# Performance work log

Hardware: AMD Instinct MI355X
Metric: run time of the kernel (lower is better)

Reference implementation:

```python
import jax, jax.numpy as jnp
import numpy as np

N, T, F_IN = 20000, 8, 64
FILTERS, HEADS = 32, 4
E = 320000
LEAKY = 0.2  # PyG GATConv default negative_slope
HID = HEADS * FILTERS  # 128


def setup_inputs() -> dict:
    key = jax.random.key(0)
    ks = jax.random.split(key, 16)
    g = lambda k, shape, scale: jax.random.normal(k, shape, dtype=jnp.float32) * scale
    return {
        "x": g(ks[0], (N, T, F_IN), 1.0),
        "edge_index": jax.random.randint(ks[1], (2, E), 0, N, dtype=jnp.int32),
        # GATConv 1: lin weight, attention vectors (per head), bias
        "W1": g(ks[2], (HID, F_IN), (2.0 / F_IN) ** 0.5),
        "att_src1": g(ks[3], (HEADS, FILTERS), 0.1),
        "att_dst1": g(ks[4], (HEADS, FILTERS), 0.1),
        "b1": jnp.zeros((HID,), jnp.float32),
        # GATConv 2
        "W2": g(ks[5], (HID, HID), (2.0 / HID) ** 0.5),
        "att_src2": g(ks[6], (HEADS, FILTERS), 0.1),
        "att_dst2": g(ks[7], (HEADS, FILTERS), 0.1),
        "b2": jnp.zeros((HID,), jnp.float32),
        # MLP head
        "lw1": g(ks[8], (FILTERS, HID), (2.0 / HID) ** 0.5),
        "lb1": jnp.zeros((FILTERS,), jnp.float32),
        "lw2": g(ks[9], (1, FILTERS), (2.0 / FILTERS) ** 0.5),
        "lb2": jnp.zeros((1,), jnp.float32),
    }


def gat_layer(x, src, dst, W, a_src, a_dst, b):
    """PyG GATConv (concat=True, add_self_loops already applied to src/dst)."""
    h = (x @ W.T).reshape(N, HEADS, FILTERS)          # [N,H,F]
    es = (h * a_src).sum(-1)                          # [N,H] per-node src score
    ed = (h * a_dst).sum(-1)                          # [N,H] per-node dst score
    e = jax.nn.leaky_relu(es[src] + ed[dst], LEAKY)   # [E',H]
    # segment softmax over incoming edges per destination node
    m = jax.ops.segment_max(e, dst, num_segments=N)
    ex = jnp.exp(e - m[dst])
    denom = jax.ops.segment_sum(ex, dst, num_segments=N)
    alpha = ex / (denom[dst] + 1e-16)                 # [E',H]
    out = jax.ops.segment_sum(h[src] * alpha[:, :, None], dst, num_segments=N)
    return out.reshape(N, HID) + b


def reference(x, edge_index, W1, att_src1, att_dst1, b1,
              W2, att_src2, att_dst2, b2, lw1, lb1, lw2, lb2):
    # add self loops (PyG GATConv default add_self_loops=True)
    loop = jnp.arange(N, dtype=edge_index.dtype)
    src = jnp.concatenate([edge_index[0], loop])
    dst = jnp.concatenate([edge_index[1], loop])

    def step(_, x_t):
        h = jax.nn.elu(gat_layer(x_t, src, dst, W1, att_src1, att_dst1, b1))
        # dropout is identity in eval mode
        h = jax.nn.elu(gat_layer(h, src, dst, W2, att_src2, att_dst2, b2))
        h = jax.nn.relu(h @ lw1.T + lb1)
        y = h @ lw2.T + lb2                            # [N,1]
        return None, y

    _, ys = jax.lax.scan(step, None, jnp.transpose(x, (1, 0, 2)))  # scan over T
    return ys  # [T, N, 1] (stacked version of the original list of outputs)
```

## Files before the change

### kernel.cpp

```cpp
#include <hip/hip_runtime.h>

constexpr int cN     = 20000;
constexpr int cT     = 8;
constexpr int cFIN   = 64;
constexpr int cHEADS = 4;
constexpr int cF     = 32;
constexpr int cHID   = 128;
constexpr int cE     = 320000;
constexpr int cET    = cE + cN;
constexpr int cR     = cN * cT;
constexpr float cLEAKY = 0.2f;
constexpr float cL2E = 1.44269504088896340736f;

typedef __attribute__((ext_vector_type(8))) short bf16x8;
typedef __attribute__((ext_vector_type(4))) float f32x4;

static __device__ __forceinline__ unsigned short f2bfu(float f) {
    unsigned int u;
    __builtin_memcpy(&u, &f, 4);
    u += 0x7FFFu + ((u >> 16) & 1u);
    return (unsigned short)(u >> 16);
}
static __device__ __forceinline__ void unpack2(unsigned int v, float& lo, float& hi) {
    unsigned int ul = v << 16, uh = v & 0xFFFF0000u;
    __builtin_memcpy(&lo, &ul, 4);
    __builtin_memcpy(&hi, &uh, 4);
}
static __device__ __forceinline__ unsigned int pack2(float lo, float hi) {
    unsigned int ul, uh;
    __builtin_memcpy(&ul, &lo, 4);
    __builtin_memcpy(&uh, &hi, 4);
    ul += 0x7FFFu + ((ul >> 16) & 1u);
    uh += 0x7FFFu + ((uh >> 16) & 1u);
    return (ul >> 16) | (uh & 0xFFFF0000u);
}

__global__ void cvt_w_kernel(const float* W1, const float* W2, const float* lw1,
                             unsigned short* W1b, unsigned short* W2b, unsigned short* lw1b) {
    int i = blockIdx.x * 256 + threadIdx.x;
    if (i < cHID * cFIN)                      W1b[i] = f2bfu(W1[i]);
    else if (i < cHID * cFIN + cHID * cHID)   W2b[i - cHID * cFIN] = f2bfu(W2[i - cHID * cFIN]);
    else if (i < cHID * cFIN + cHID * cHID + cF * cHID)
        lw1b[i - cHID * cFIN - cHID * cHID] = f2bfu(lw1[i - cHID * cFIN - cHID * cHID]);
}

__global__ void deg_init_kernel(int* deg) {
    int n = blockIdx.x * blockDim.x + threadIdx.x;
    if (n < cN) deg[n] = 1;
}
__global__ void deg_count_kernel(const int* ei, int* deg) {
    int e = blockIdx.x * blockDim.x + threadIdx.x;
    if (e < cE) atomicAdd(&deg[ei[cE + e]], 1);
}
__global__ void scan_kernel(const int* deg, int* offs, int* cur) {
    __shared__ int sdeg[79 * 256];
    __shared__ int lds[256];
    int tid = threadIdx.x;
    #pragma unroll 4
    for (int k = 0; k < 79; k++) {
        int idx = k * 256 + tid;
        sdeg[idx] = (idx < cN) ? deg[idx] : 0;
    }
    __syncthreads();
    const int CH = 79;
    int base = tid * CH;
    int tot = 0;
    #pragma unroll 8
    for (int j = 0; j < CH; j++) tot += sdeg[base + j];
    lds[tid] = tot;
    __syncthreads();
    for (int off = 1; off < 256; off <<= 1) {
        int v = (tid >= off) ? lds[tid - off] : 0;
        __syncthreads();
        lds[tid] += v;
        __syncthreads();
    }
    int run = lds[tid] - tot;
    for (int j = 0; j < CH; j++) {
        int idx = base + j;
        if (idx < cN) { offs[idx] = run; cur[idx] = run; run += sdeg[idx]; }
    }
    if (tid == 255) offs[cN] = lds[255];
}
__global__ void scatter_kernel(const int* ei, int* cur, int* csr) {
    int e = blockIdx.x * blockDim.x + threadIdx.x;
    if (e >= cET) return;
    int s, d;
    if (e < cE) { s = ei[e]; d = ei[cE + e]; }
    else        { s = e - cE; d = s; }
    int pos = atomicAdd(&cur[d], 1);
    csr[pos] = s;
}

__global__ __launch_bounds__(256) void gemm1_fused_kernel(
        const float* __restrict__ x, const unsigned short* __restrict__ W,
        const float* __restrict__ a_src, const float* __restrict__ a_dst,
        unsigned short* __restrict__ hb, float* __restrict__ es, float* __restrict__ ed) {
    __shared__ float hl[64][132];
    int tid  = threadIdx.x;
    int wave = tid >> 6;
    int lane = tid & 63;
    int q    = lane >> 4;
    int mi   = lane & 15;
    int m0   = blockIdx.x * 64 + wave * 16;

    int rho = m0 + mi;
    int t = rho / cN;
    int n = rho - t * cN;
    const float* xr = x + (size_t)n * (cT * cFIN) + t * cFIN;

    bf16x8 afrag[2];
    #pragma unroll
    for (int s = 0; s < 2; s++) {
        float4 v0 = *(const float4*)(xr + s * 32 + q * 8);
        float4 v1 = *(const float4*)(xr + s * 32 + q * 8 + 4);
        bf16x8 f;
        f[0] = (short)f2bfu(v0.x); f[1] = (short)f2bfu(v0.y);
        f[2] = (short)f2bfu(v0.z); f[3] = (short)f2bfu(v0.w);
        f[4] = (short)f2bfu(v1.x); f[5] = (short)f2bfu(v1.y);
        f[6] = (short)f2bfu(v1.z); f[7] = (short)f2bfu(v1.w);
        afrag[s] = f;
    }

    f32x4 acc[8];
    #pragma unroll
    for (int ct = 0; ct < 8; ct++) acc[ct] = (f32x4){0.f, 0.f, 0.f, 0.f};
    #pragma unroll
    for (int ct = 0; ct < 8; ct++) {
        int c = ct * 16 + mi;
        #pragma unroll
        for (int s = 0; s < 2; s++) {
            bf16x8 bfrag = *(const bf16x8*)(W + (size_t)c * cFIN + s * 32 + q * 8);
            acc[ct] = __builtin_amdgcn_mfma_f32_16x16x32_bf16(afrag[s], bfrag, acc[ct], 0, 0, 0);
        }
    }

    #pragma unroll
    for (int ct = 0; ct < 8; ct++)
        #pragma unroll
        for (int r = 0; r < 4; r++)
            hl[wave * 16 + q * 4 + r][ct * 16 + mi] = acc[ct][r];
    __syncthreads();

    {
        int r2 = tid & 63;
        int hd = tid >> 6;
        int rg = blockIdx.x * 64 + r2;
        const float* hr = &hl[r2][hd * cF];
        const float* sa = a_src + hd * cF;
        const float* da = a_dst + hd * cF;
        float s1 = 0.f, s2 = 0.f;
        #pragma unroll 8
        for (int f = 0; f < cF; f++) {
            float hv = hr[f];
            s1 += hv * sa[f];
            s2 += hv * da[f];
        }
        es[rg * cHEADS + hd] = s1 * cL2E;
        ed[rg * cHEADS + hd] = s2 * cL2E;
    }

    size_t base = (size_t)blockIdx.x * 64 * cHID;
    #pragma unroll
    for (int it = 0; it < 8; it++) {
        int g   = tid + it * 256;
        int row = g >> 5;
        int c4  = (g & 31) * 4;
        float4 v = *(const float4*)&hl[row][c4];
        unsigned int p0 = pack2(v.x, v.y), p1 = pack2(v.z, v.w);
        *(uint2*)(hb + base + (size_t)row * cHID + c4) = make_uint2(p0, p1);
    }
}

static __device__ __forceinline__ void agg_core(
        const unsigned short* __restrict__ hb, const float* __restrict__ es,
        const float* __restrict__ ed, const int* __restrict__ offs,
        const int* __restrict__ csr, const float* __restrict__ bias,
        int t, int n, int j, float* r) {
    int head = j >> 2;
    int rho  = t * cN + n;
    int s0 = offs[n], s1 = offs[n + 1];
    float edn = ed[(size_t)rho * cHEADS + head];
    const char* hpc = (const char*)(hb + (size_t)t * cN * cHID);
    const char* epc = (const char*)(es + (size_t)t * cN * cHEADS);
    const char* cc  = (const char*)csr;
    unsigned jo = (unsigned)j * 16u;
    unsigned ho = (unsigned)head * 4u;

    float acc[8] = {};
    float den = 0.f;
    int i = s0;
    for (; i + 3 < s1; i += 4) {
        unsigned io = (unsigned)i * 4u;
        int sa = *(const int*)(cc + io);
        int sb = *(const int*)(cc + io + 4u);
        int sc = *(const int*)(cc + io + 8u);
        int sd = *(const int*)(cc + io + 12u);
        uint4 ra = *(const uint4*)(hpc + (((unsigned)sa) << 8) + jo);
        uint4 rb = *(const uint4*)(hpc + (((unsigned)sb) << 8) + jo);
        uint4 rc = *(const uint4*)(hpc + (((unsigned)sc) << 8) + jo);
        uint4 rd = *(const uint4*)(hpc + (((unsigned)sd) << 8) + jo);
        float ea = *(const float*)(epc + (((unsigned)sa) << 4) + ho) + edn;
        float eb = *(const float*)(epc + (((unsigned)sb) << 4) + ho) + edn;
        float ec = *(const float*)(epc + (((unsigned)sc) << 4) + ho) + edn;
        float ee = *(const float*)(epc + (((unsigned)sd) << 4) + ho) + edn;
        ea = (ea >= 0.f) ? ea : cLEAKY * ea;
        eb = (eb >= 0.f) ? eb : cLEAKY * eb;
        ec = (ec >= 0.f) ? ec : cLEAKY * ec;
        ee = (ee >= 0.f) ? ee : cLEAKY * ee;
        float wa = __builtin_amdgcn_exp2f(ea), wb = __builtin_amdgcn_exp2f(eb);
        float wc = __builtin_amdgcn_exp2f(ec), wd = __builtin_amdgcn_exp2f(ee);
        den += wa; den += wb; den += wc; den += wd;
        float lo, hi;
        unpack2(ra.x, lo, hi); acc[0] += wa * lo; acc[1] += wa * hi;
        unpack2(ra.y, lo, hi); acc[2] += wa * lo; acc[3] += wa * hi;
        unpack2(ra.z, lo, hi); acc[4] += wa * lo; acc[5] += wa * hi;
        unpack2(ra.w, lo, hi); acc[6] += wa * lo; acc[7] += wa * hi;
        unpack2(rb.x, lo, hi); acc[0] += wb * lo; acc[1] += wb * hi;
        unpack2(rb.y, lo, hi); acc[2] += wb * lo; acc[3] += wb * hi;
        unpack2(rb.z, lo, hi); acc[4] += wb * lo; acc[5] += wb * hi;
        unpack2(rb.w, lo, hi); acc[6] += wb * lo; acc[7] += wb * hi;
        unpack2(rc.x, lo, hi); acc[0] += wc * lo; acc[1] += wc * hi;
        unpack2(rc.y, lo, hi); acc[2] += wc * lo; acc[3] += wc * hi;
        unpack2(rc.z, lo, hi); acc[4] += wc * lo; acc[5] += wc * hi;
        unpack2(rc.w, lo, hi); acc[6] += wc * lo; acc[7] += wc * hi;
        unpack2(rd.x, lo, hi); acc[0] += wd * lo; acc[1] += wd * hi;
        unpack2(rd.y, lo, hi); acc[2] += wd * lo; acc[3] += wd * hi;
        unpack2(rd.z, lo, hi); acc[4] += wd * lo; acc[5] += wd * hi;
        unpack2(rd.w, lo, hi); acc[6] += wd * lo; acc[7] += wd * hi;
    }
    for (; i < s1; i++) {
        int sa = *(const int*)(cc + (unsigned)i * 4u);
        uint4 ra = *(const uint4*)(hpc + (((unsigned)sa) << 8) + jo);
        float ea = *(const float*)(epc + (((unsigned)sa) << 4) + ho) + edn;
        ea = (ea >= 0.f) ? ea : cLEAKY * ea;
        float wa = __builtin_amdgcn_exp2f(ea);
        den += wa;
        float lo, hi;
        unpack2(ra.x, lo, hi); acc[0] += wa * lo; acc[1] += wa * hi;
        unpack2(ra.y, lo, hi); acc[2] += wa * lo; acc[3] += wa * hi;
        unpack2(ra.z, lo, hi); acc[4] += wa * lo; acc[5] += wa * hi;
        unpack2(ra.w, lo, hi); acc[6] += wa * lo; acc[7] += wa * hi;
    }
    float inv = 1.f / (den + 1e-16f);
    float4 b0 = *(const float4*)(bias + 8 * j);
    float4 b1v = *(const float4*)(bias + 8 * j + 4);
    float v0 = acc[0] * inv + b0.x;  r[0] = (v0 > 0.f) ? v0 : expm1f(v0);
    float v1 = acc[1] * inv + b0.y;  r[1] = (v1 > 0.f) ? v1 : expm1f(v1);
    float v2 = acc[2] * inv + b0.z;  r[2] = (v2 > 0.f) ? v2 : expm1f(v2);
    float v3 = acc[3] * inv + b0.w;  r[3] = (v3 > 0.f) ? v3 : expm1f(v3);
    float v4 = acc[4] * inv + b1v.x; r[4] = (v4 > 0.f) ? v4 : expm1f(v4);
    float v5 = acc[5] * inv + b1v.y; r[5] = (v5 > 0.f) ? v5 : expm1f(v5);
    float v6 = acc[6] * inv + b1v.z; r[6] = (v6 > 0.f) ? v6 : expm1f(v6);
    float v7 = acc[7] * inv + b1v.w; r[7] = (v7 > 0.f) ? v7 : expm1f(v7);
}

__global__ __launch_bounds__(256) void agg_gemm_kernel(
        const unsigned short* __restrict__ hb, const float* __restrict__ es,
        const float* __restrict__ ed, const int* __restrict__ offs,
        const int* __restrict__ csr, const float* __restrict__ bias,
        const unsigned short* __restrict__ W2, const float* __restrict__ a_src,
        const float* __restrict__ a_dst, unsigned short* __restrict__ hb2,
        float* __restrict__ es2, float* __restrict__ ed2) {
    __shared__ unsigned short tile[16 * 128];
    __shared__ float hl[16][132];
    int b    = blockIdx.x;
    int t    = b & 7;
    int g    = b >> 3;
    int tid  = threadIdx.x;
    int lrow = tid >> 4;
    int j    = tid & 15;
    int n0   = g * 16;

    float r[8];
    agg_core(hb, es, ed, offs, csr, bias, t, n0 + lrow, j, r);
    {
        uint4 o;
        o.x = pack2(r[0], r[1]); o.y = pack2(r[2], r[3]);
        o.z = pack2(r[4], r[5]); o.w = pack2(r[6], r[7]);
        unsigned tb = (unsigned)lrow * 256u + (((unsigned)j * 16u) ^ (((unsigned)(lrow & 7)) << 4));
        *(uint4*)((char*)tile + tb) = o;
    }
    __syncthreads();

    int wave = tid >> 6;
    int lane = tid & 63;
    int q    = lane >> 4;
    int mi   = lane & 15;
    bf16x8 afrag[4];
    #pragma unroll
    for (int s = 0; s < 4; s++) {
        unsigned addr = (unsigned)mi * 256u +
                        (((unsigned)(s * 64 + q * 16)) ^ (((unsigned)(mi & 7)) << 4));
        afrag[s] = *(const bf16x8*)((const char*)tile + addr);
    }
    f32x4 acc2[2];
    acc2[0] = (f32x4){0.f, 0.f, 0.f, 0.f};
    acc2[1] = (f32x4){0.f, 0.f, 0.f, 0.f};
    #pragma unroll
    for (int ct = 0; ct < 2; ct++) {
        int c = (wave * 2 + ct) * 16 + mi;
        #pragma unroll
        for (int s = 0; s < 4; s++) {
            bf16x8 bfrag = *(const bf16x8*)(W2 + (size_t)c * cHID + s * 32 + q * 8);
            acc2[ct] = __builtin_amdgcn_mfma_f32_16x16x32_bf16(afrag[s], bfrag, acc2[ct], 0, 0, 0);
        }
    }
    #pragma unroll
    for (int ct = 0; ct < 2; ct++)
        #pragma unroll
        for (int rr = 0; rr < 4; rr++)
            hl[q * 4 + rr][(wave * 2 + ct) * 16 + mi] = acc2[ct][rr];
    __syncthreads();

    if (tid < 64) {
        int r2 = tid & 15;
        int hd = tid >> 4;
        int rg = t * cN + n0 + r2;
        const float* hr = &hl[r2][hd * cF];
        const float* sa = a_src + hd * cF;
        const float* da = a_dst + hd * cF;
        float s1 = 0.f, s2 = 0.f;
        #pragma unroll 8
        for (int f = 0; f < cF; f++) {
            float hv = hr[f];
            s1 += hv * sa[f];
            s2 += hv * da[f];
        }
        es2[(size_t)rg * cHEADS + hd] = s1 * cL2E;
        ed2[(size_t)rg * cHEADS + hd] = s2 * cL2E;
    }
    {
        int row = tid >> 4;
        int c8  = (tid & 15) * 8;
        float4 v0 = *(const float4*)&hl[row][c8];
        float4 v1 = *(const float4*)&hl[row][c8 + 4];
        uint4 o;
        o.x = pack2(v0.x, v0.y); o.y = pack2(v0.z, v0.w);
        o.z = pack2(v1.x, v1.y); o.w = pack2(v1.z, v1.w);
        *(uint4*)(hb2 + (size_t)(t * cN + n0 + row) * cHID + c8) = o;
    }
}

__global__ __launch_bounds__(256) void TemporalGAT_20005957665499_kernel(
        const unsigned short* __restrict__ hb2, const float* __restrict__ es,
        const float* __restrict__ ed, const int* __restrict__ offs,
        const int* __restrict__ csr, const float* __restrict__ bias,
        const unsigned short* __restrict__ lw1b, const float* __restrict__ lb1,
        const float* __restrict__ lw2, const float* __restrict__ lb2,
        float* __restrict__ out) {
    __shared__ unsigned short tile[16 * 128];
    int b    = blockIdx.x;
    int t    = b & 7;
    int g    = b >> 3;
    int tid  = threadIdx.x;
    int lrow = tid >> 4;
    int j    = tid & 15;
    int n0   = g * 16;

    float r[8];
    agg_core(hb2, es, ed, offs, csr, bias, t, n0 + lrow, j, r);
    {
        uint4 o;
        o.x = pack2(r[0], r[1]); o.y = pack2(r[2], r[3]);
        o.z = pack2(r[4], r[5]); o.w = pack2(r[6], r[7]);
        unsigned tb = (unsigned)lrow * 256u + (((unsigned)j * 16u) ^ (((unsigned)(lrow & 7)) << 4));
        *(uint4*)((char*)tile + tb) = o;
    }
    __syncthreads();

    if (tid < 64) {
        int q  = tid >> 4;
        int mi = tid & 15;
        bf16x8 afrag[4];
        #pragma unroll
        for (int s = 0; s < 4; s++) {
            unsigned addr = (unsigned)mi * 256u +
                            (((unsigned)(s * 64 + q * 16)) ^ (((unsigned)(mi & 7)) << 4));
            afrag[s] = *(const bf16x8*)((const char*)tile + addr);
        }
        f32x4 acc2[2];
        acc2[0] = (f32x4){0.f, 0.f, 0.f, 0.f};
        acc2[1] = (f32x4){0.f, 0.f, 0.f, 0.f};
        #pragma unroll
        for (int ct = 0; ct < 2; ct++) {
            int c = ct * 16 + mi;
            #pragma unroll
            for (int s = 0; s < 4; s++) {
                bf16x8 bfrag = *(const bf16x8*)(lw1b + (size_t)c * cHID + s * 32 + q * 8);
                acc2[ct] = __builtin_amdgcn_mfma_f32_16x16x32_bf16(afrag[s], bfrag, acc2[ct], 0, 0, 0);
            }
        }
        float lb1a = lb1[mi], lb1b_ = lb1[16 + mi];
        float lw2a = lw2[mi], lw2b_ = lw2[16 + mi];
        float l2 = lb2[0];
        #pragma unroll
        for (int rr = 0; rr < 4; rr++) {
            float va = fmaxf(acc2[0][rr] + lb1a, 0.f);
            float vb = fmaxf(acc2[1][rr] + lb1b_, 0.f);
            float v = va * lw2a + vb * lw2b_;
            v += __shfl_xor(v, 1);
            v += __shfl_xor(v, 2);
            v += __shfl_xor(v, 4);
            v += __shfl_xor(v, 8);
            if (mi == 0) out[t * cN + n0 + q * 4 + rr] = v + l2;
        }
    }
}

extern "C" void kernel_launch(void* const* d_in, const int* in_sizes, int n_in,
                              void* d_out, int out_size, void* d_ws, size_t ws_size,
                              hipStream_t stream) {
    const float* x   = (const float*)d_in[0];
    const int*   ei  = (const int*)d_in[1];
    const float* W1  = (const float*)d_in[2];
    const float* as1 = (const float*)d_in[3];
    const float* ad1 = (const float*)d_in[4];
    const float* b1  = (const float*)d_in[5];
    const float* W2  = (const float*)d_in[6];
    const float* as2 = (const float*)d_in[7];
    const float* ad2 = (const float*)d_in[8];
    const float* b2  = (const float*)d_in[9];
    const float* lw1 = (const float*)d_in[10];
    const float* lb1 = (const float*)d_in[11];
    const float* lw2 = (const float*)d_in[12];
    const float* lb2 = (const float*)d_in[13];
    float* out = (float*)d_out;
    (void)in_sizes; (void)n_in; (void)out_size; (void)ws_size;

    char* ws = (char*)d_ws;
    size_t o = 0;
    auto carveN = [&](size_t bytes) { void* p = ws + o; o += (bytes + 255) & ~(size_t)255; return p; };
    unsigned short* hb   = (unsigned short*)carveN((size_t)cR * cHID * 2);
    unsigned short* hb2  = (unsigned short*)carveN((size_t)cR * cHID * 2);
    unsigned short* W1b  = (unsigned short*)carveN((size_t)cHID * cFIN * 2);
    unsigned short* W2b  = (unsigned short*)carveN((size_t)cHID * cHID * 2);
    unsigned short* lw1b = (unsigned short*)carveN((size_t)cF * cHID * 2);
    float* es1_buf = (float*)carveN((size_t)cR * cHEADS * 4);
    float* ed1_buf = (float*)carveN((size_t)cR * cHEADS * 4);
    float* es2_buf = (float*)carveN((size_t)cR * cHEADS * 4);
    float* ed2_buf = (float*)carveN((size_t)cR * cHEADS * 4);
    int*   deg     = (int*)carveN((size_t)cN * 4);
    int*   offs    = (int*)carveN((size_t)(cN + 1) * 4);
    int*   cursor  = (int*)carveN((size_t)cN * 4);
    int*   csr     = (int*)carveN((size_t)cET * 4);

    cvt_w_kernel<<<(cHID * cFIN + cHID * cHID + cF * cHID + 255) / 256, 256, 0, stream>>>(
        W1, W2, lw1, W1b, W2b, lw1b);

    deg_init_kernel<<<(cN + 255) / 256, 256, 0, stream>>>(deg);
    deg_count_kernel<<<(cE + 255) / 256, 256, 0, stream>>>(ei, deg);
    scan_kernel<<<1, 256, 0, stream>>>(deg, offs, cursor);
    scatter_kernel<<<(cET + 255) / 256, 256, 0, stream>>>(ei, cursor, csr);

    gemm1_fused_kernel<<<cR / 64, 256, 0, stream>>>(x, W1b, as1, ad1, hb, es1_buf, ed1_buf);
    agg_gemm_kernel<<<(cN / 16) * cT, 256, 0, stream>>>(
        hb, es1_buf, ed1_buf, offs, csr, b1, W2b, as2, ad2, hb2, es2_buf, ed2_buf);
    TemporalGAT_20005957665499_kernel<<<(cN / 16) * cT, 256, 0, stream>>>(
        hb2, es2_buf, ed2_buf, offs, csr, b2, lw1b, lb1, lw2, lb2, out);
}
```

Before: 382.8 us.

## Aggregate 16 features per thread with 32-node blocks and merge setup kernels

```diff
diff --git a/kernel.cpp b/kernel.cpp
--- a/kernel.cpp
+++ b/kernel.cpp
@@ -14,6 +14,7 @@
 
 typedef __attribute__((ext_vector_type(8))) short bf16x8;
 typedef __attribute__((ext_vector_type(4))) float f32x4;
+typedef __attribute__((ext_vector_type(2))) float f32x2;
 
 static __device__ __forceinline__ unsigned short f2bfu(float f) {
     unsigned int u;
@@ -21,10 +22,12 @@
     u += 0x7FFFu + ((u >> 16) & 1u);
     return (unsigned short)(u >> 16);
 }
-static __device__ __forceinline__ void unpack2(unsigned int v, float& lo, float& hi) {
+static __device__ __forceinline__ f32x2 bfp2(unsigned int v) {
     unsigned int ul = v << 16, uh = v & 0xFFFF0000u;
+    float lo, hi;
     __builtin_memcpy(&lo, &ul, 4);
     __builtin_memcpy(&hi, &uh, 4);
+    return (f32x2){lo, hi};
 }
 static __device__ __forceinline__ unsigned int pack2(float lo, float hi) {
     unsigned int ul, uh;
@@ -34,24 +37,25 @@
     uh += 0x7FFFu + ((uh >> 16) & 1u);
     return (ul >> 16) | (uh & 0xFFFF0000u);
 }
-
-__global__ void cvt_w_kernel(const float* W1, const float* W2, const float* lw1,
-                             unsigned short* W1b, unsigned short* W2b, unsigned short* lw1b) {
+static __device__ __forceinline__ void fma16(uint4 r0, uint4 r1, float w, f32x2* acc) {
+    f32x2 w2 = (f32x2){w, w};
+    acc[0] += w2 * bfp2(r0.x); acc[1] += w2 * bfp2(r0.y);
+    acc[2] += w2 * bfp2(r0.z); acc[3] += w2 * bfp2(r0.w);
+    acc[4] += w2 * bfp2(r1.x); acc[5] += w2 * bfp2(r1.y);
+    acc[6] += w2 * bfp2(r1.z); acc[7] += w2 * bfp2(r1.w);
+}
+
+__global__ void cvt_deg_kernel(const float* W1, const float* W2, const float* lw1,
+                               const int* ei, unsigned short* W1b, unsigned short* W2b,
+                               unsigned short* lw1b, int* deg) {
     int i = blockIdx.x * 256 + threadIdx.x;
     if (i < cHID * cFIN)                      W1b[i] = f2bfu(W1[i]);
     else if (i < cHID * cFIN + cHID * cHID)   W2b[i - cHID * cFIN] = f2bfu(W2[i - cHID * cFIN]);
     else if (i < cHID * cFIN + cHID * cHID + cF * cHID)
         lw1b[i - cHID * cFIN - cHID * cHID] = f2bfu(lw1[i - cHID * cFIN - cHID * cHID]);
-}
-
-__global__ void deg_init_kernel(int* deg) {
-    int n = blockIdx.x * blockDim.x + threadIdx.x;
-    if (n < cN) deg[n] = 1;
-}
-__global__ void deg_count_kernel(const int* ei, int* deg) {
-    int e = blockIdx.x * blockDim.x + threadIdx.x;
-    if (e < cE) atomicAdd(&deg[ei[cE + e]], 1);
-}
+    if (i < cE) atomicAdd(&deg[ei[cE + i]], 1);
+}
+
 __global__ void scan_kernel(const int* deg, int* offs, int* cur) {
     __shared__ int sdeg[79 * 256];
     __shared__ int lds[256];
@@ -59,7 +63,7 @@
     #pragma unroll 4
     for (int k = 0; k < 79; k++) {
         int idx = k * 256 + tid;
-        sdeg[idx] = (idx < cN) ? deg[idx] : 0;
+        sdeg[idx] = (idx < cN) ? deg[idx] + 1 : 0;
     }
     __syncthreads();
     const int CH = 79;
@@ -172,87 +176,78 @@
     }
 }
 
-static __device__ __forceinline__ void agg_core(
+static __device__ __forceinline__ void agg_core16(
         const unsigned short* __restrict__ hb, const float* __restrict__ es,
         const float* __restrict__ ed, const int* __restrict__ offs,
         const int* __restrict__ csr, const float* __restrict__ bias,
         int t, int n, int j, float* r) {
-    int head = j >> 2;
-    int rho  = t * cN + n;
+    int head = j >> 1;
     int s0 = offs[n], s1 = offs[n + 1];
-    float edn = ed[(size_t)rho * cHEADS + head];
-    const char* hpc = (const char*)(hb + (size_t)t * cN * cHID);
-    const char* epc = (const char*)(es + (size_t)t * cN * cHEADS);
-    const char* cc  = (const char*)csr;
-    unsigned jo = (unsigned)j * 16u;
+    float edn = ed[(size_t)(t * cN + n) * cHEADS + head];
+    const char* hp = (const char*)(hb + (size_t)t * cN * cHID);
+    const char* ep = (const char*)(es + (size_t)t * cN * cHEADS);
+    const char* cc = (const char*)csr;
+    unsigned jo = (unsigned)j * 32u;
     unsigned ho = (unsigned)head * 4u;
 
-    float acc[8] = {};
+    f32x2 acc[8];
+    #pragma unroll
+    for (int k = 0; k < 8; k++) acc[k] = (f32x2){0.f, 0.f};
     float den = 0.f;
     int i = s0;
-    for (; i + 3 < s1; i += 4) {
+    for (; i + 1 < s1; i += 2) {
         unsigned io = (unsigned)i * 4u;
         int sa = *(const int*)(cc + io);
         int sb = *(const int*)(cc + io + 4u);
-        int sc = *(const int*)(cc + io + 8u);
-        int sd = *(const int*)(cc + io + 12u);
-        uint4 ra = *(const uint4*)(hpc + (((unsigned)sa) << 8) + jo);
-        uint4 rb = *(const uint4*)(hpc + (((unsigned)sb) << 8) + jo);
-        uint4 rc = *(const uint4*)(hpc + (((unsigned)sc) << 8) + jo);
-        uint4 rd = *(const uint4*)(hpc + (((unsigned)sd) << 8) + jo);
-        float ea = *(const float*)(epc + (((unsigned)sa) << 4) + ho) + edn;
-        float eb = *(const float*)(epc + (((unsigned)sb) << 4) + ho) + edn;
-        float ec = *(const float*)(epc + (((unsigned)sc) << 4) + ho) + edn;
-        float ee = *(const float*)(epc + (((unsigned)sd) << 4) + ho) + edn;
+        unsigned oa = ((unsigned)sa) << 8, ob = ((unsigned)sb) << 8;
+        uint4 ra0 = *(const uint4*)(hp + oa + jo);
+        uint4 ra1 = *(const uint4*)(hp + oa + jo + 16u);
+        uint4 rb0 = *(const uint4*)(hp + ob + jo);
+        uint4 rb1 = *(const uint4*)(hp + ob + jo + 16u);
+        float ea = *(const float*)(ep + (((unsigned)sa) << 4) + ho) + edn;
+        float eb = *(const float*)(ep + (((unsigned)sb) << 4) + ho) + edn;
         ea = (ea >= 0.f) ? ea : cLEAKY * ea;
         eb = (eb >= 0.f) ? eb : cLEAKY * eb;
-        ec = (ec >= 0.f) ? ec : cLEAKY * ec;
-        ee = (ee >= 0.f) ? ee : cLEAKY * ee;
-        float wa = __builtin_amdgcn_exp2f(ea), wb = __builtin_amdgcn_exp2f(eb);
-        float wc = __builtin_amdgcn_exp2f(ec), wd = __builtin_amdgcn_exp2f(ee);
-        den += wa; den += wb; den += wc; den += wd;
-        float lo, hi;
-        unpack2(ra.x, lo, hi); acc[0] += wa * lo; acc[1] += wa * hi;
-        unpack2(ra.y, lo, hi); acc[2] += wa * lo; acc[3] += wa * hi;
-        unpack2(ra.z, lo, hi); acc[4] += wa * lo; acc[5] += wa * hi;
-        unpack2(ra.w, lo, hi); acc[6] += wa * lo; acc[7] += wa * hi;
-        unpack2(rb.x, lo, hi); acc[0] += wb * lo; acc[1] += wb * hi;
-        unpack2(rb.y, lo, hi); acc[2] += wb * lo; acc[3] += wb * hi;
-        unpack2(rb.z, lo, hi); acc[4] += wb * lo; acc[5] += wb * hi;
-        unpack2(rb.w, lo, hi); acc[6] += wb * lo; acc[7] += wb * hi;
-        unpack2(rc.x, lo, hi); acc[0] += wc * lo; acc[1] += wc * hi;
-        unpack2(rc.y, lo, hi); acc[2] += wc * lo; acc[3] += wc * hi;
-        unpack2(rc.z, lo, hi); acc[4] += wc * lo; acc[5] += wc * hi;
-        unpack2(rc.w, lo, hi); acc[6] += wc * lo; acc[7] += wc * hi;
-        unpack2(rd.x, lo, hi); acc[0] += wd * lo; acc[1] += wd * hi;
-        unpack2(rd.y, lo, hi); acc[2] += wd * lo; acc[3] += wd * hi;
-        unpack2(rd.z, lo, hi); acc[4] += wd * lo; acc[5] += wd * hi;
-        unpack2(rd.w, lo, hi); acc[6] += wd * lo; acc[7] += wd * hi;
+        float wa = __builtin_amdgcn_exp2f(ea);
+        float wb = __builtin_amdgcn_exp2f(eb);
+        den += wa; den += wb;
+        fma16(ra0, ra1, wa, acc);
+        fma16(rb0, rb1, wb, acc);
     }
     for (; i < s1; i++) {
         int sa = *(const int*)(cc + (unsigned)i * 4u);
-        uint4 ra = *(const uint4*)(hpc + (((unsigned)sa) << 8) + jo);
-        float ea = *(const float*)(epc + (((unsigned)sa) << 4) + ho) + edn;
+        unsigned oa = ((unsigned)sa) << 8;
+        uint4 ra0 = *(const uint4*)(hp + oa + jo);
+        uint4 ra1 = *(const uint4*)(hp + oa + jo + 16u);
+        float ea = *(const float*)(ep + (((unsigned)sa) << 4) + ho) + edn;
         ea = (ea >= 0.f) ? ea : cLEAKY * ea;
         float wa = __builtin_amdgcn_exp2f(ea);
         den += wa;
-        float lo, hi;
-        unpack2(ra.x, lo, hi); acc[0] += wa * lo; acc[1] += wa * hi;
-        unpack2(ra.y, lo, hi); acc[2] += wa * lo; acc[3] += wa * hi;
-        unpack2(ra.z, lo, hi); acc[4] += wa * lo; acc[5] += wa * hi;
-        unpack2(ra.w, lo, hi); acc[6] += wa * lo; acc[7] += wa * hi;
+        fma16(ra0, ra1, wa, acc);
     }
     float inv = 1.f / (den + 1e-16f);
-    float4 b0 = *(const float4*)(bias + 8 * j);
-    float4 b1v = *(const float4*)(bias + 8 * j + 4);
-    float v0 = acc[0] * inv + b0.x;  r[0] = (v0 > 0.f) ? v0 : expm1f(v0);
-    float v1 = acc[1] * inv + b0.y;  r[1] = (v1 > 0.f) ? v1 : expm1f(v1);
-    float v2 = acc[2] * inv + b0.z;  r[2] = (v2 > 0.f) ? v2 : expm1f(v2);
-    float v3 = acc[3] * inv + b0.w;  r[3] = (v3 > 0.f) ? v3 : expm1f(v3);
-    float v4 = acc[4] * inv + b1v.x; r[4] = (v4 > 0.f) ? v4 : expm1f(v4);
-    float v5 = acc[5] * inv + b1v.y; r[5] = (v5 > 0.f) ? v5 : expm1f(v5);
-    float v6 = acc[6] * inv + b1v.z; r[6] = (v6 > 0.f) ? v6 : expm1f(v6);
-    float v7 = acc[7] * inv + b1v.w; r[7] = (v7 > 0.f) ? v7 : expm1f(v7);
+    const float* bp = bias + 16 * j;
+    #pragma unroll
+    for (int k = 0; k < 8; k++) {
+        float v0 = acc[k].x * inv + bp[2 * k];
+        float v1 = acc[k].y * inv + bp[2 * k + 1];
+        r[2 * k]     = (v0 > 0.f) ? v0 : expm1f(v0);
+        r[2 * k + 1] = (v1 > 0.f) ? v1 : expm1f(v1);
+    }
+}
+
+static __device__ __forceinline__ void tile_write16(unsigned short* tile, int row, int j,
+                                                    const float* r) {
+    uint4 o0, o1;
+    o0.x = pack2(r[0], r[1]);  o0.y = pack2(r[2], r[3]);
+    o0.z = pack2(r[4], r[5]);  o0.w = pack2(r[6], r[7]);
+    o1.x = pack2(r[8], r[9]);  o1.y = pack2(r[10], r[11]);
+    o1.z = pack2(r[12], r[13]); o1.w = pack2(r[14], r[15]);
+    unsigned swz = ((unsigned)(row & 7)) << 4;
+    unsigned jo  = (unsigned)j * 32u;
+    char* base = (char*)tile + (unsigned)row * 256u;
+    *(uint4*)(base + (jo ^ swz)) = o0;
+    *(uint4*)(base + ((jo + 16u) ^ swz)) = o1;
 }
 
 __global__ __launch_bounds__(256) void agg_gemm_kernel(
@@ -262,44 +257,41 @@
         const unsigned short* __restrict__ W2, const float* __restrict__ a_src,
         const float* __restrict__ a_dst, unsigned short* __restrict__ hb2,
         float* __restrict__ es2, float* __restrict__ ed2) {
-    __shared__ unsigned short tile[16 * 128];
-    __shared__ float hl[16][132];
+    __shared__ unsigned short tile[32 * 128];
+    __shared__ float hl[2][16][132];
     int b    = blockIdx.x;
     int t    = b & 7;
     int g    = b >> 3;
     int tid  = threadIdx.x;
-    int lrow = tid >> 4;
-    int j    = tid & 15;
-    int n0   = g * 16;
-
-    float r[8];
-    agg_core(hb, es, ed, offs, csr, bias, t, n0 + lrow, j, r);
-    {
-        uint4 o;
-        o.x = pack2(r[0], r[1]); o.y = pack2(r[2], r[3]);
-        o.z = pack2(r[4], r[5]); o.w = pack2(r[6], r[7]);
-        unsigned tb = (unsigned)lrow * 256u + (((unsigned)j * 16u) ^ (((unsigned)(lrow & 7)) << 4));
-        *(uint4*)((char*)tile + tb) = o;
-    }
+    int row  = tid >> 3;
+    int j    = tid & 7;
+    int n0   = g * 32;
+    int n    = n0 + row;
+
+    float r[16];
+    agg_core16(hb, es, ed, offs, csr, bias, t, n, j, r);
+    tile_write16(tile, row, j, r);
     __syncthreads();
 
     int wave = tid >> 6;
     int lane = tid & 63;
     int q    = lane >> 4;
     int mi   = lane & 15;
+    int p    = wave >> 1;
+    int ch   = wave & 1;
     bf16x8 afrag[4];
     #pragma unroll
     for (int s = 0; s < 4; s++) {
-        unsigned addr = (unsigned)mi * 256u +
+        unsigned addr = (unsigned)(p * 16 + mi) * 256u +
                         (((unsigned)(s * 64 + q * 16)) ^ (((unsigned)(mi & 7)) << 4));
         afrag[s] = *(const bf16x8*)((const char*)tile + addr);
     }
-    f32x4 acc2[2];
-    acc2[0] = (f32x4){0.f, 0.f, 0.f, 0.f};
-    acc2[1] = (f32x4){0.f, 0.f, 0.f, 0.f};
-    #pragma unroll
-    for (int ct = 0; ct < 2; ct++) {
-        int c = (wave * 2 + ct) * 16 + mi;
+    f32x4 acc2[4];
+    #pragma unroll
+    for (int ct = 0; ct < 4; ct++) acc2[ct] = (f32x4){0.f, 0.f, 0.f, 0.f};
+    #pragma unroll
+    for (int ct = 0; ct < 4; ct++) {
+        int c = (ch * 4 + ct) * 16 + mi;
         #pragma unroll
         for (int s = 0; s < 4; s++) {
             bf16x8 bfrag = *(const bf16x8*)(W2 + (size_t)c * cHID + s * 32 + q * 8);
@@ -307,17 +299,18 @@
         }
     }
     #pragma unroll
-    for (int ct = 0; ct < 2; ct++)
+    for (int ct = 0; ct < 4; ct++)
         #pragma unroll
         for (int rr = 0; rr < 4; rr++)
-            hl[q * 4 + rr][(wave * 2 + ct) * 16 + mi] = acc2[ct][rr];
-    __syncthreads();
-
-    if (tid < 64) {
+            hl[p][q * 4 + rr][(ch * 4 + ct) * 16 + mi] = acc2[ct][rr];
+    __syncthreads();
+
+    if (tid < 128) {
+        int pp = tid >> 6;
         int r2 = tid & 15;
-        int hd = tid >> 4;
-        int rg = t * cN + n0 + r2;
-        const float* hr = &hl[r2][hd * cF];
+        int hd = (tid >> 4) & 3;
+        int rg = t * cN + n0 + pp * 16 + r2;
+        const float* hr = &hl[pp][r2][hd * cF];
         const float* sa = a_src + hd * cF;
         const float* da = a_dst + hd * cF;
         float s1 = 0.f, s2 = 0.f;
@@ -330,15 +323,16 @@
         es2[(size_t)rg * cHEADS + hd] = s1 * cL2E;
         ed2[(size_t)rg * cHEADS + hd] = s2 * cL2E;
     }
-    {
-        int row = tid >> 4;
-        int c8  = (tid & 15) * 8;
-        float4 v0 = *(const float4*)&hl[row][c8];
-        float4 v1 = *(const float4*)&hl[row][c8 + 4];
+    #pragma unroll
+    for (int pp = 0; pp < 2; pp++) {
+        int rw = tid >> 4;
+        int c8 = (tid & 15) * 8;
+        float4 v0 = *(const float4*)&hl[pp][rw][c8];
+        float4 v1 = *(const float4*)&hl[pp][rw][c8 + 4];
         uint4 o;
         o.x = pack2(v0.x, v0.y); o.y = pack2(v0.z, v0.w);
         o.z = pack2(v1.x, v1.y); o.w = pack2(v1.z, v1.w);
-        *(uint4*)(hb2 + (size_t)(t * cN + n0 + row) * cHID + c8) = o;
+        *(uint4*)(hb2 + (size_t)(t * cN + n0 + pp * 16 + rw) * cHID + c8) = o;
     }
 }
 
@@ -349,39 +343,37 @@
         const unsigned short* __restrict__ lw1b, const float* __restrict__ lb1,
         const float* __restrict__ lw2, const float* __restrict__ lb2,
         float* __restrict__ out) {
-    __shared__ unsigned short tile[16 * 128];
+    __shared__ unsigned short tile[32 * 128];
     int b    = blockIdx.x;
     int t    = b & 7;
     int g    = b >> 3;
     int tid  = threadIdx.x;
-    int lrow = tid >> 4;
-    int j    = tid & 15;
-    int n0   = g * 16;
-
-    float r[8];
-    agg_core(hb2, es, ed, offs, csr, bias, t, n0 + lrow, j, r);
-    {
-        uint4 o;
-        o.x = pack2(r[0], r[1]); o.y = pack2(r[2], r[3]);
-        o.z = pack2(r[4], r[5]); o.w = pack2(r[6], r[7]);
-        unsigned tb = (unsigned)lrow * 256u + (((unsigned)j * 16u) ^ (((unsigned)(lrow & 7)) << 4));
-        *(uint4*)((char*)tile + tb) = o;
-    }
-    __syncthreads();
-
-    if (tid < 64) {
-        int q  = tid >> 4;
-        int mi = tid & 15;
+    int row  = tid >> 3;
+    int j    = tid & 7;
+    int n0   = g * 32;
+    int n    = n0 + row;
+
+    float r[16];
+    agg_core16(hb2, es, ed, offs, csr, bias, t, n, j, r);
+    tile_write16(tile, row, j, r);
+    __syncthreads();
+
+    int wave = tid >> 6;
+    if (wave < 2) {
+        int p  = wave;
+        int lane = tid & 63;
+        int q  = lane >> 4;
+        int mi = lane & 15;
         bf16x8 afrag[4];
         #pragma unroll
         for (int s = 0; s < 4; s++) {
-            unsigned addr = (unsigned)mi * 256u +
+            unsigned addr = (unsigned)(p * 16 + mi) * 256u +
                             (((unsigned)(s * 64 + q * 16)) ^ (((unsigned)(mi & 7)) << 4));
             afrag[s] = *(const bf16x8*)((const char*)tile + addr);
         }
         f32x4 acc2[2];
         acc2[0] = (f32x4){0.f, 0.f, 0.f, 0.f};
-        acc2[1] = (f32x4){0.f, 0.f, 0.f, 0.f};
+        acc2[1] = acc2[0];
         #pragma unroll
         for (int ct = 0; ct < 2; ct++) {
             int c = ct * 16 + mi;
@@ -403,7 +395,7 @@
             v += __shfl_xor(v, 2);
             v += __shfl_xor(v, 4);
             v += __shfl_xor(v, 8);
-            if (mi == 0) out[t * cN + n0 + q * 4 + rr] = v + l2;
+            if (mi == 0) out[t * cN + n0 + p * 16 + q * 4 + rr] = v + l2;
         }
     }
 }
@@ -445,17 +437,14 @@
     int*   cursor  = (int*)carveN((size_t)cN * 4);
     int*   csr     = (int*)carveN((size_t)cET * 4);
 
-    cvt_w_kernel<<<(cHID * cFIN + cHID * cHID + cF * cHID + 255) / 256, 256, 0, stream>>>(
-        W1, W2, lw1, W1b, W2b, lw1b);
-
-    deg_init_kernel<<<(cN + 255) / 256, 256, 0, stream>>>(deg);
-    deg_count_kernel<<<(cE + 255) / 256, 256, 0, stream>>>(ei, deg);
+    hipMemsetAsync(deg, 0, (size_t)cN * 4, stream);
+    cvt_deg_kernel<<<(cE + 255) / 256, 256, 0, stream>>>(W1, W2, lw1, ei, W1b, W2b, lw1b, deg);
     scan_kernel<<<1, 256, 0, stream>>>(deg, offs, cursor);
     scatter_kernel<<<(cET + 255) / 256, 256, 0, stream>>>(ei, cursor, csr);
 
     gemm1_fused_kernel<<<cR / 64, 256, 0, stream>>>(x, W1b, as1, ad1, hb, es1_buf, ed1_buf);
-    agg_gemm_kernel<<<(cN / 16) * cT, 256, 0, stream>>>(
+    agg_gemm_kernel<<<(cN / 32) * cT, 256, 0, stream>>>(
         hb, es1_buf, ed1_buf, offs, csr, b1, W2b, as2, ad2, hb2, es2_buf, ed2_buf);
-    TemporalGAT_20005957665499_kernel<<<(cN / 16) * cT, 256, 0, stream>>>(
+    TemporalGAT_20005957665499_kernel<<<(cN / 32) * cT, 256, 0, stream>>>(
         hb2, es2_buf, ed2_buf, offs, csr, b2, lw1b, lb1, lw2, lb2, out);
 }
```

Measured after the change: 414.2 us. 1.08x slower.

## Store hidden features in permuted layout, drop LDS staging, fuse weight conversion with degree count

Applied to the files above, without the earlier changes.

```diff
diff --git a/kernel.cpp b/kernel.cpp
--- a/kernel.cpp
+++ b/kernel.cpp
@@ -12,6 +12,7 @@
 constexpr float cLEAKY = 0.2f;
 constexpr float cL2E = 1.44269504088896340736f;
 
+
 typedef __attribute__((ext_vector_type(8))) short bf16x8;
 typedef __attribute__((ext_vector_type(4))) float f32x4;
 
@@ -34,24 +35,35 @@
     uh += 0x7FFFu + ((uh >> 16) & 1u);
     return (ul >> 16) | (uh & 0xFFFF0000u);
 }
-
-__global__ void cvt_w_kernel(const float* W1, const float* W2, const float* lw1,
-                             unsigned short* W1b, unsigned short* W2b, unsigned short* lw1b) {
+static __device__ __forceinline__ int featOf(int p) {
+    return ((p >> 5) << 5) + ((p >> 1) & 15) + ((p & 1) << 4);
+}
+
+__global__ void cvt_deg_kernel(const float* W1, const float* W2, const float* lw1,
+                               const float* b1, const float* b2, const int* ei,
+                               unsigned short* W1b, unsigned short* W2bP,
+                               unsigned short* lw1bP, float* b1P, float* b2P, int* deg) {
     int i = blockIdx.x * 256 + threadIdx.x;
-    if (i < cHID * cFIN)                      W1b[i] = f2bfu(W1[i]);
-    else if (i < cHID * cFIN + cHID * cHID)   W2b[i - cHID * cFIN] = f2bfu(W2[i - cHID * cFIN]);
-    else if (i < cHID * cFIN + cHID * cHID + cF * cHID)
-        lw1b[i - cHID * cFIN - cHID * cHID] = f2bfu(lw1[i - cHID * cFIN - cHID * cHID]);
-}
-
-__global__ void deg_init_kernel(int* deg) {
-    int n = blockIdx.x * blockDim.x + threadIdx.x;
-    if (n < cN) deg[n] = 1;
-}
-__global__ void deg_count_kernel(const int* ei, int* deg) {
-    int e = blockIdx.x * blockDim.x + threadIdx.x;
-    if (e < cE) atomicAdd(&deg[ei[cE + e]], 1);
-}
+    if (i < 8192) {
+        W1b[i] = f2bfu(W1[i]);
+    } else if (i < 8192 + 16384) {
+        int jj = i - 8192;
+        int c = jj >> 7, p = jj & 127;
+        W2bP[jj] = f2bfu(W2[c * cHID + featOf(p)]);
+    } else if (i < 8192 + 16384 + 4096) {
+        int jj = i - 8192 - 16384;
+        int c = jj >> 7, p = jj & 127;
+        lw1bP[jj] = f2bfu(lw1[c * cHID + featOf(p)]);
+    } else if (i < 8192 + 16384 + 4096 + 128) {
+        int p = i - 8192 - 16384 - 4096;
+        b1P[p] = b1[featOf(p)];
+    } else if (i < 8192 + 16384 + 4096 + 256) {
+        int p = i - 8192 - 16384 - 4096 - 128;
+        b2P[p] = b2[featOf(p)];
+    }
+    if (i < cE) atomicAdd(&deg[ei[cE + i]], 1);
+}
+
 __global__ void scan_kernel(const int* deg, int* offs, int* cur) {
     __shared__ int sdeg[79 * 256];
     __shared__ int lds[256];
@@ -59,7 +71,7 @@
     #pragma unroll 4
     for (int k = 0; k < 79; k++) {
         int idx = k * 256 + tid;
-        sdeg[idx] = (idx < cN) ? deg[idx] : 0;
+        sdeg[idx] = (idx < cN) ? deg[idx] + 1 : 0;
     }
     __syncthreads();
     const int CH = 79;
@@ -96,7 +108,6 @@
         const float* __restrict__ x, const unsigned short* __restrict__ W,
         const float* __restrict__ a_src, const float* __restrict__ a_dst,
         unsigned short* __restrict__ hb, float* __restrict__ es, float* __restrict__ ed) {
-    __shared__ float hl[64][132];
     int tid  = threadIdx.x;
     int wave = tid >> 6;
     int lane = tid & 63;
@@ -136,39 +147,34 @@
     }
 
     #pragma unroll
-    for (int ct = 0; ct < 8; ct++)
-        #pragma unroll
-        for (int r = 0; r < 4; r++)
-            hl[wave * 16 + q * 4 + r][ct * 16 + mi] = acc[ct][r];
-    __syncthreads();
-
-    {
-        int r2 = tid & 63;
-        int hd = tid >> 6;
-        int rg = blockIdx.x * 64 + r2;
-        const float* hr = &hl[r2][hd * cF];
-        const float* sa = a_src + hd * cF;
-        const float* da = a_dst + hd * cF;
-        float s1 = 0.f, s2 = 0.f;
-        #pragma unroll 8
-        for (int f = 0; f < cF; f++) {
-            float hv = hr[f];
-            s1 += hv * sa[f];
-            s2 += hv * da[f];
-        }
-        es[rg * cHEADS + hd] = s1 * cL2E;
-        ed[rg * cHEADS + hd] = s2 * cL2E;
-    }
-
-    size_t base = (size_t)blockIdx.x * 64 * cHID;
-    #pragma unroll
-    for (int it = 0; it < 8; it++) {
-        int g   = tid + it * 256;
-        int row = g >> 5;
-        int c4  = (g & 31) * 4;
-        float4 v = *(const float4*)&hl[row][c4];
-        unsigned int p0 = pack2(v.x, v.y), p1 = pack2(v.z, v.w);
-        *(uint2*)(hb + base + (size_t)row * cHID + c4) = make_uint2(p0, p1);
+    for (int h = 0; h < 4; h++) {
+        float a0 = a_src[h * 32 + mi], a1 = a_src[h * 32 + 16 + mi];
+        float d0 = a_dst[h * 32 + mi], d1 = a_dst[h * 32 + 16 + mi];
+        #pragma unroll
+        for (int rr = 0; rr < 4; rr++) {
+            float vs = acc[2 * h][rr] * a0 + acc[2 * h + 1][rr] * a1;
+            float vd = acc[2 * h][rr] * d0 + acc[2 * h + 1][rr] * d1;
+            vs += __shfl_xor(vs, 1); vs += __shfl_xor(vs, 2);
+            vs += __shfl_xor(vs, 4); vs += __shfl_xor(vs, 8);
+            vd += __shfl_xor(vd, 1); vd += __shfl_xor(vd, 2);
+            vd += __shfl_xor(vd, 4); vd += __shfl_xor(vd, 8);
+            if (mi == 0) {
+                int rg = m0 + q * 4 + rr;
+                es[rg * cHEADS + h] = vs * cL2E;
+                ed[rg * cHEADS + h] = vd * cL2E;
+            }
+        }
+    }
+
+    #pragma unroll
+    for (int rr = 0; rr < 4; rr++) {
+        int rg = m0 + q * 4 + rr;
+        unsigned short* hrow = hb + (size_t)rg * cHID;
+        #pragma unroll
+        for (int h = 0; h < 4; h++) {
+            unsigned pv = pack2(acc[2 * h][rr], acc[2 * h + 1][rr]);
+            *(unsigned*)(hrow + h * 32 + mi * 2) = pv;
+        }
     }
 }
 
@@ -258,12 +264,11 @@
 __global__ __launch_bounds__(256) void agg_gemm_kernel(
         const unsigned short* __restrict__ hb, const float* __restrict__ es,
         const float* __restrict__ ed, const int* __restrict__ offs,
-        const int* __restrict__ csr, const float* __restrict__ bias,
-        const unsigned short* __restrict__ W2, const float* __restrict__ a_src,
+        const int* __restrict__ csr, const float* __restrict__ b1P,
+        const unsigned short* __restrict__ W2bP, const float* __restrict__ a_src,
         const float* __restrict__ a_dst, unsigned short* __restrict__ hb2,
         float* __restrict__ es2, float* __restrict__ ed2) {
     __shared__ unsigned short tile[16 * 128];
-    __shared__ float hl[16][132];
     int b    = blockIdx.x;
     int t    = b & 7;
     int g    = b >> 3;
@@ -273,7 +278,7 @@
     int n0   = g * 16;
 
     float r[8];
-    agg_core(hb, es, ed, offs, csr, bias, t, n0 + lrow, j, r);
+    agg_core(hb, es, ed, offs, csr, b1P, t, n0 + lrow, j, r);
     {
         uint4 o;
         o.x = pack2(r[0], r[1]); o.y = pack2(r[2], r[3]);
@@ -296,57 +301,49 @@
     }
     f32x4 acc2[2];
     acc2[0] = (f32x4){0.f, 0.f, 0.f, 0.f};
-    acc2[1] = (f32x4){0.f, 0.f, 0.f, 0.f};
+    acc2[1] = acc2[0];
     #pragma unroll
     for (int ct = 0; ct < 2; ct++) {
         int c = (wave * 2 + ct) * 16 + mi;
         #pragma unroll
         for (int s = 0; s < 4; s++) {
-            bf16x8 bfrag = *(const bf16x8*)(W2 + (size_t)c * cHID + s * 32 + q * 8);
+            bf16x8 bfrag = *(const bf16x8*)(W2bP + (size_t)c * cHID + s * 32 + q * 8);
             acc2[ct] = __builtin_amdgcn_mfma_f32_16x16x32_bf16(afrag[s], bfrag, acc2[ct], 0, 0, 0);
         }
     }
-    #pragma unroll
-    for (int ct = 0; ct < 2; ct++)
-        #pragma unroll
-        for (int rr = 0; rr < 4; rr++)
-            hl[q * 4 + rr][(wave * 2 + ct) * 16 + mi] = acc2[ct][rr];
-    __syncthreads();
-
-    if (tid < 64) {
-        int r2 = tid & 15;
-        int hd = tid >> 4;
-        int rg = t * cN + n0 + r2;
-        const float* hr = &hl[r2][hd * cF];
-        const float* sa = a_src + hd * cF;
-        const float* da = a_dst + hd * cF;
-        float s1 = 0.f, s2 = 0.f;
-        #pragma unroll 8
-        for (int f = 0; f < cF; f++) {
-            float hv = hr[f];
-            s1 += hv * sa[f];
-            s2 += hv * da[f];
-        }
-        es2[(size_t)rg * cHEADS + hd] = s1 * cL2E;
-        ed2[(size_t)rg * cHEADS + hd] = s2 * cL2E;
-    }
+
     {
-        int row = tid >> 4;
-        int c8  = (tid & 15) * 8;
-        float4 v0 = *(const float4*)&hl[row][c8];
-        float4 v1 = *(const float4*)&hl[row][c8 + 4];
-        uint4 o;
-        o.x = pack2(v0.x, v0.y); o.y = pack2(v0.z, v0.w);
-        o.z = pack2(v1.x, v1.y); o.w = pack2(v1.z, v1.w);
-        *(uint4*)(hb2 + (size_t)(t * cN + n0 + row) * cHID + c8) = o;
+        float a0 = a_src[wave * 32 + mi], a1 = a_src[wave * 32 + 16 + mi];
+        float d0 = a_dst[wave * 32 + mi], d1 = a_dst[wave * 32 + 16 + mi];
+        #pragma unroll
+        for (int rr = 0; rr < 4; rr++) {
+            float vs = acc2[0][rr] * a0 + acc2[1][rr] * a1;
+            float vd = acc2[0][rr] * d0 + acc2[1][rr] * d1;
+            vs += __shfl_xor(vs, 1); vs += __shfl_xor(vs, 2);
+            vs += __shfl_xor(vs, 4); vs += __shfl_xor(vs, 8);
+            vd += __shfl_xor(vd, 1); vd += __shfl_xor(vd, 2);
+            vd += __shfl_xor(vd, 4); vd += __shfl_xor(vd, 8);
+            if (mi == 0) {
+                int rg = t * cN + n0 + q * 4 + rr;
+                es2[(size_t)rg * cHEADS + wave] = vs * cL2E;
+                ed2[(size_t)rg * cHEADS + wave] = vd * cL2E;
+            }
+        }
+    }
+
+    #pragma unroll
+    for (int rr = 0; rr < 4; rr++) {
+        int rg = t * cN + n0 + q * 4 + rr;
+        unsigned pv = pack2(acc2[0][rr], acc2[1][rr]);
+        *(unsigned*)(hb2 + (size_t)rg * cHID + wave * 32 + mi * 2) = pv;
     }
 }
 
 __global__ __launch_bounds__(256) void TemporalGAT_20005957665499_kernel(
         const unsigned short* __restrict__ hb2, const float* __restrict__ es,
         const float* __restrict__ ed, const int* __restrict__ offs,
-        const int* __restrict__ csr, const float* __restrict__ bias,
-        const unsigned short* __restrict__ lw1b, const float* __restrict__ lb1,
+        const int* __restrict__ csr, const float* __restrict__ b2P,
+        const unsigned short* __restrict__ lw1bP, const float* __restrict__ lb1,
         const float* __restrict__ lw2, const float* __restrict__ lb2,
         float* __restrict__ out) {
     __shared__ unsigned short tile[16 * 128];
@@ -359,7 +356,7 @@
     int n0   = g * 16;
 
     float r[8];
-    agg_core(hb2, es, ed, offs, csr, bias, t, n0 + lrow, j, r);
+    agg_core(hb2, es, ed, offs, csr, b2P, t, n0 + lrow, j, r);
     {
         uint4 o;
         o.x = pack2(r[0], r[1]); o.y = pack2(r[2], r[3]);
@@ -381,13 +378,13 @@
         }
         f32x4 acc2[2];
         acc2[0] = (f32x4){0.f, 0.f, 0.f, 0.f};
-        acc2[1] = (f32x4){0.f, 0.f, 0.f, 0.f};
+        acc2[1] = acc2[0];
         #pragma unroll
         for (int ct = 0; ct < 2; ct++) {
             int c = ct * 16 + mi;
             #pragma unroll
             for (int s = 0; s < 4; s++) {
-                bf16x8 bfrag = *(const bf16x8*)(lw1b + (size_t)c * cHID + s * 32 + q * 8);
+                bf16x8 bfrag = *(const bf16x8*)(lw1bP + (size_t)c * cHID + s * 32 + q * 8);
                 acc2[ct] = __builtin_amdgcn_mfma_f32_16x16x32_bf16(afrag[s], bfrag, acc2[ct], 0, 0, 0);
             }
         }
@@ -431,11 +428,13 @@
     char* ws = (char*)d_ws;
     size_t o = 0;
     auto carveN = [&](size_t bytes) { void* p = ws + o; o += (bytes + 255) & ~(size_t)255; return p; };
-    unsigned short* hb   = (unsigned short*)carveN((size_t)cR * cHID * 2);
-    unsigned short* hb2  = (unsigned short*)carveN((size_t)cR * cHID * 2);
-    unsigned short* W1b  = (unsigned short*)carveN((size_t)cHID * cFIN * 2);
-    unsigned short* W2b  = (unsigned short*)carveN((size_t)cHID * cHID * 2);
-    unsigned short* lw1b = (unsigned short*)carveN((size_t)cF * cHID * 2);
+    unsigned short* hb    = (unsigned short*)carveN((size_t)cR * cHID * 2);
+    unsigned short* hb2   = (unsigned short*)carveN((size_t)cR * cHID * 2);
+    unsigned short* W1b   = (unsigned short*)carveN((size_t)cHID * cFIN * 2);
+    unsigned short* W2bP  = (unsigned short*)carveN((size_t)cHID * cHID * 2);
+    unsigned short* lw1bP = (unsigned short*)carveN((size_t)cF * cHID * 2);
+    float* b1P     = (float*)carveN((size_t)cHID * 4);
+    float* b2P     = (float*)carveN((size_t)cHID * 4);
     float* es1_buf = (float*)carveN((size_t)cR * cHEADS * 4);
     float* ed1_buf = (float*)carveN((size_t)cR * cHEADS * 4);
     float* es2_buf = (float*)carveN((size_t)cR * cHEADS * 4);
@@ -445,17 +444,15 @@
     int*   cursor  = (int*)carveN((size_t)cN * 4);
     int*   csr     = (int*)carveN((size_t)cET * 4);
 
-    cvt_w_kernel<<<(cHID * cFIN + cHID * cHID + cF * cHID + 255) / 256, 256, 0, stream>>>(
-        W1, W2, lw1, W1b, W2b, lw1b);
-
-    deg_init_kernel<<<(cN + 255) / 256, 256, 0, stream>>>(deg);
-    deg_count_kernel<<<(cE + 255) / 256, 256, 0, stream>>>(ei, deg);
+    hipMemsetAsync(deg, 0, (size_t)cN * 4, stream);
+    cvt_deg_kernel<<<(cE + 255) / 256, 256, 0, stream>>>(
+        W1, W2, lw1, b1, b2, ei, W1b, W2bP, lw1bP, b1P, b2P, deg);
     scan_kernel<<<1, 256, 0, stream>>>(deg, offs, cursor);
     scatter_kernel<<<(cET + 255) / 256, 256, 0, stream>>>(ei, cursor, csr);
 
     gemm1_fused_kernel<<<cR / 64, 256, 0, stream>>>(x, W1b, as1, ad1, hb, es1_buf, ed1_buf);
     agg_gemm_kernel<<<(cN / 16) * cT, 256, 0, stream>>>(
-        hb, es1_buf, ed1_buf, offs, csr, b1, W2b, as2, ad2, hb2, es2_buf, ed2_buf);
+        hb, es1_buf, ed1_buf, offs, csr, b1P, W2bP, as2, ad2, hb2, es2_buf, ed2_buf);
     TemporalGAT_20005957665499_kernel<<<(cN / 16) * cT, 256, 0, stream>>>(
-        hb2, es2_buf, ed2_buf, offs, csr, b2, lw1b, lb1, lw2, lb2, out);
-}
+        hb2, es2_buf, ed2_buf, offs, csr, b2P, lw1bP, lb1, lw2, lb2, out);
+}
```

Result: no change. 387.5 us (+1.2%).
